# Kernel tuning notes

Measured on AMD Instinct MI355X. Metric: run time of the kernel, lower is better.

The kernel has to match this reference:

```python
import jax, jax.numpy as jnp
import numpy as np

N_NODES = 100000
N_EDGES = 1250000
D_FEAT = 64


def setup_inputs() -> dict:
    key = jax.random.key(0)
    kx, ke = jax.random.split(key)
    x = jax.random.normal(kx, (N_NODES, D_FEAT), dtype=jnp.float32)
    edge_index = jax.random.randint(ke, (2, N_EDGES), 0, N_NODES, dtype=jnp.int64)
    return {"x": x, "edge_index": edge_index}


def _aggregate(x, src, dst, num_nodes):
    # out[i] = sum_{e: dst[e]==i} x[src[e]]  (identity message, 'add' aggr)
    return jax.ops.segment_sum(x[src], dst, num_segments=num_nodes)


def reference(x, edge_index):
    num_nodes = x.shape[0]
    src, dst = edge_index[0], edge_index[1]  # PyG source_to_target flow
    h = _aggregate(x, src, dst, num_nodes)   # conv1
    h = jax.nn.relu(h)
    h = _aggregate(h, src, dst, num_nodes)   # conv2
    return h
```

## Files before the change

### kernel.cpp

```cpp
#include <hip/hip_runtime.h>
#include <hip/hip_bf16.h>


#define N_FEAT   64
#define B_SHIFT  6
#define NPB      64
#define CAPB     1024
#define HALF_CAP 512
#define NLOC     32
#define NB_H     1568
#define GSTRIDE  16
#define TILE     4096

typedef unsigned int u32;
typedef unsigned short u16;
typedef __attribute__((ext_vector_type(8))) unsigned short u16x8;
typedef __attribute__((ext_vector_type(4))) unsigned int u32x4;
typedef __attribute__((ext_vector_type(2))) float f32x2;

__device__ inline u16 f2bf(float f) {
    u32 u = __builtin_bit_cast(u32, f);
    return (u16)((u + 0x7FFFu + ((u >> 16) & 1u)) >> 16);
}

__global__ __launch_bounds__(256) void partition_convert_kernel(
    const float* __restrict__ xf, u16* __restrict__ xb, int n_elems,
    const int* __restrict__ src, const int* __restrict__ dst,
    u32* __restrict__ gcur,
    u32* __restrict__ bdata,
    int n_edges, int n_buckets, int part_blocks)
{
    __shared__ u32 hist[NB_H];
    __shared__ u32 wcur[NB_H];

    const int tid = threadIdx.x;

    if ((int)blockIdx.x >= part_blocks) {
        int i = (((int)blockIdx.x - part_blocks) * 256 + tid) * 8;
        if (i < n_elems) {
            float4 a = *(const float4*)(xf + i);
            float4 b = *(const float4*)(xf + i + 4);
            u16x8 r;
            r[0]=f2bf(a.x); r[1]=f2bf(a.y); r[2]=f2bf(a.z); r[3]=f2bf(a.w);
            r[4]=f2bf(b.x); r[5]=f2bf(b.y); r[6]=f2bf(b.z); r[7]=f2bf(b.w);
            *(u16x8*)(xb + i) = r;
        }
        return;
    }

    const int tbase = (int)blockIdx.x * TILE;
    const int tend  = min(tbase + TILE, n_edges);

    for (int i = tid; i < NB_H; i += 256) hist[i] = 0;
    __syncthreads();

    for (int e = tbase + tid; e < tend; e += 256)
        atomicAdd(&hist[(u32)dst[e] >> B_SHIFT], 1u);
    __syncthreads();

    for (int b = tid; b < n_buckets; b += 256) {
        u32 h = hist[b];
        if (h) wcur[b] = atomicAdd(&gcur[b * GSTRIDE], h);
    }
    __syncthreads();

    for (int e = tbase + tid; e < tend; e += 256) {
        int d = dst[e];
        int s = src[e];
        u32 b   = (u32)d >> B_SHIFT;
        u32 pos = atomicAdd(&wcur[b], 1u);
        if (pos < CAPB)
            bdata[(size_t)b * CAPB + pos] = ((u32)(d & (NPB - 1)) << 17) | (u32)s;
    }
}

__global__ __launch_bounds__(256) void aggregate_kernel(
    const u16* __restrict__ xin,
    const u32* __restrict__ gcur,
    const u32* __restrict__ bdata,
    u16* __restrict__ out_bf,
    float* __restrict__ out_f,
    int n_nodes, int pass)
{
    __shared__ u32 ebuf[HALF_CAP];
    __shared__ u32 sorted[HALF_CAP];
    __shared__ u32 lcnt[NLOC];
    __shared__ u32 lpos[NLOC];
    __shared__ int ptr[NLOC + 1];
    __shared__ u32 ecnt;

    const int tid  = threadIdx.x;
    const int B    = blockIdx.x >> 1;
    const int half = blockIdx.x & 1;

    if (tid < NLOC) { lcnt[tid] = 0; lpos[tid] = 0; }
    if (tid == 0) ecnt = 0;
    __syncthreads();

    int cnt = (int)gcur[B * GSTRIDE];
    if (cnt > CAPB) cnt = CAPB;

    const u32* bd = bdata + (size_t)B * CAPB;
    for (int j = tid; j < cnt; j += 256) {
        u32 p  = bd[j];
        int dl = (int)(p >> 17);
        if ((dl >> 5) == half) {
            u32 pos = atomicAdd(&ecnt, 1u);
            if (pos < HALF_CAP) {
                ebuf[pos] = p;
                atomicAdd(&lcnt[dl & (NLOC - 1)], 1u);
            }
        }
    }
    __syncthreads();

    if (tid < NLOC) {
        int sc = (int)lcnt[tid];
        #pragma unroll
        for (int d = 1; d < NLOC; d <<= 1) {
            int o = __shfl_up(sc, d);
            if (tid >= d) sc += o;
        }
        ptr[tid + 1] = sc;
        if (tid == 0) ptr[0] = 0;
    }
    __syncthreads();

    int en = (int)ecnt; if (en > HALF_CAP) en = HALF_CAP;
    for (int j = tid; j < en; j += 256) {
        u32 p  = ebuf[j];
        int dl = (int)(p >> 17) & (NLOC - 1);
        u32 pos = atomicAdd(&lpos[dl], 1u);
        sorted[ptr[dl] + pos] = p & 0x1FFFFu;
    }
    __syncthreads();

    const int w    = tid >> 6;
    const int lane = tid & 63;
    const int grp  = lane >> 3;
    const int sub  = lane & 7;
    const char* xc = (const char*)xin;

    const int nl   = w * 8 + grp;
    const int node = B * NPB + half * NLOC + nl;
    const int s0 = ptr[nl], s1 = ptr[nl + 1];

    f32x2 a0={0.f,0.f}, a1={0.f,0.f}, a2={0.f,0.f}, a3={0.f,0.f};
    for (int j = s0; j < s1; ++j) {
        u32 s = sorted[j];
        u32x4 v = *(const u32x4*)(xc + ((size_t)s << 7) + (sub << 4));
        a0 += (f32x2){ __builtin_bit_cast(float, v[0] << 16),
                       __builtin_bit_cast(float, v[0] & 0xFFFF0000u) };
        a1 += (f32x2){ __builtin_bit_cast(float, v[1] << 16),
                       __builtin_bit_cast(float, v[1] & 0xFFFF0000u) };
        a2 += (f32x2){ __builtin_bit_cast(float, v[2] << 16),
                       __builtin_bit_cast(float, v[2] & 0xFFFF0000u) };
        a3 += (f32x2){ __builtin_bit_cast(float, v[3] << 16),
                       __builtin_bit_cast(float, v[3] & 0xFFFF0000u) };
    }

    if (node < n_nodes) {
        if (pass == 0) {
            u16x8 o;
            o[0]=f2bf(fmaxf(a0.x,0.f)); o[1]=f2bf(fmaxf(a0.y,0.f));
            o[2]=f2bf(fmaxf(a1.x,0.f)); o[3]=f2bf(fmaxf(a1.y,0.f));
            o[4]=f2bf(fmaxf(a2.x,0.f)); o[5]=f2bf(fmaxf(a2.y,0.f));
            o[6]=f2bf(fmaxf(a3.x,0.f)); o[7]=f2bf(fmaxf(a3.y,0.f));
            *(u16x8*)(out_bf + (size_t)node * N_FEAT + sub * 8) = o;
        } else {
            float* dp = out_f + (size_t)node * N_FEAT + sub * 8;
            *(float4*)dp       = (float4){a0.x, a0.y, a1.x, a1.y};
            *(float4*)(dp + 4) = (float4){a2.x, a2.y, a3.x, a3.y};
        }
    }
}

extern "C" void kernel_launch(void* const* d_in, const int* in_sizes, int n_in,
                              void* d_out, int out_size, void* d_ws, size_t ws_size,
                              hipStream_t stream) {
    const float* x          = (const float*)d_in[0];
    const int*   edge_index = (const int*)d_in[1];

    const int n_edges = in_sizes[1] / 2;
    const int* src = edge_index;
    const int* dst = edge_index + n_edges;

    const int n_nodes   = out_size / N_FEAT;
    const int n_buckets = (n_nodes + NPB - 1) >> B_SHIFT;
    float* out = (float*)d_out;

    const size_t xb_bytes    = (size_t)out_size * sizeof(u16);
    const size_t hb_bytes    = (size_t)out_size * sizeof(u16);
    const size_t bdata_bytes = (size_t)n_buckets * CAPB * sizeof(u32);
    const size_t gcur_bytes  = (size_t)NB_H * GSTRIDE * sizeof(u32);

    char* w = (char*)d_ws;
    u16* xb    = (u16*)w;                w += xb_bytes;
    u16* hb    = (u16*)w;                w += hb_bytes;
    u32* bdata = (u32*)w;                w += bdata_bytes;
    u32* gcur  = (u32*)w;

    hipMemsetAsync(gcur, 0, gcur_bytes, stream);

    const int part_blocks = (n_edges + TILE - 1) / TILE;
    const int conv_blocks = (out_size / 8 + 255) / 256;
    partition_convert_kernel<<<part_blocks + conv_blocks, 256, 0, stream>>>(
        x, xb, out_size, src, dst, gcur, bdata, n_edges, n_buckets, part_blocks);

    const int agg_blocks = 2 * n_buckets;
    aggregate_kernel<<<agg_blocks, 256, 0, stream>>>(xb, gcur, bdata, hb, nullptr, n_nodes, 0);
    aggregate_kernel<<<agg_blocks, 256, 0, stream>>>(hb, gcur, bdata, nullptr, out, n_nodes, 1);
}
```

Before: 178.3 us.

## Sort edge bins once into CSR and reuse in both aggregation passes

Adds a bin_sort_kernel that sorts each 128-node bin's edges by destination once and writes per-node pointers, so both aggregation passes read a ready CSR instead of re-partitioning and sorting in shared memory each time. Bins grow to 128 nodes with larger tiles, and the global-cursor atomics are issued in a rotated order per block to spread contention. The aggregate loop loads eight source ids cooperatively and broadcasts them with shuffles. This costs an extra kernel launch and an extra pass over the edge data, and relies on the larger bin capacity of 2048 not overflowing.

```diff
diff --git a/kernel.cpp b/kernel.cpp
--- a/kernel.cpp
+++ b/kernel.cpp
@@ -2,15 +2,14 @@
 #include <hip/hip_bf16.h>
 
 
-#define N_FEAT   64
-#define B_SHIFT  6
-#define NPB      64
-#define CAPB     1024
-#define HALF_CAP 512
-#define NLOC     32
-#define NB_H     1568
-#define GSTRIDE  16
-#define TILE     4096
+#define N_FEAT    64
+#define BIN_SHIFT 7
+#define BIN_NODES 128
+#define CAPBIN    2048
+#define NB_H      784
+#define GSTRIDE   16
+#define TILE      8192
+#define NPTR      (BIN_NODES + 1)
 
 typedef unsigned int u32;
 typedef unsigned short u16;
@@ -27,8 +26,8 @@
     const float* __restrict__ xf, u16* __restrict__ xb, int n_elems,
     const int* __restrict__ src, const int* __restrict__ dst,
     u32* __restrict__ gcur,
-    u32* __restrict__ bdata,
-    int n_edges, int n_buckets, int part_blocks)
+    u32* __restrict__ cbdata,
+    int n_edges, int n_bins, int part_blocks)
 {
     __shared__ u32 hist[NB_H];
     __shared__ u32 wcur[NB_H];
@@ -55,10 +54,12 @@
     __syncthreads();
 
     for (int e = tbase + tid; e < tend; e += 256)
-        atomicAdd(&hist[(u32)dst[e] >> B_SHIFT], 1u);
-    __syncthreads();
-
-    for (int b = tid; b < n_buckets; b += 256) {
+        atomicAdd(&hist[(u32)dst[e] >> BIN_SHIFT], 1u);
+    __syncthreads();
+
+    const int rot = (int)(((u32)blockIdx.x * 193u) % (u32)n_bins);
+    for (int i = tid; i < n_bins; i += 256) {
+        int b = i + rot; if (b >= n_bins) b -= n_bins;
         u32 h = hist[b];
         if (h) wcur[b] = atomicAdd(&gcur[b * GSTRIDE], h);
     }
@@ -67,73 +68,80 @@
     for (int e = tbase + tid; e < tend; e += 256) {
         int d = dst[e];
         int s = src[e];
-        u32 b   = (u32)d >> B_SHIFT;
+        u32 b   = (u32)d >> BIN_SHIFT;
         u32 pos = atomicAdd(&wcur[b], 1u);
-        if (pos < CAPB)
-            bdata[(size_t)b * CAPB + pos] = ((u32)(d & (NPB - 1)) << 17) | (u32)s;
-    }
+        if (pos < CAPBIN)
+            cbdata[(size_t)b * CAPBIN + pos] =
+                ((u32)(d & (BIN_NODES - 1)) << 17) | (u32)s;
+    }
+}
+
+__global__ __launch_bounds__(256) void bin_sort_kernel(
+    u32* __restrict__ cbdata,
+    const u32* __restrict__ gcur,
+    u32* __restrict__ nodeptr,
+    int n_bins)
+{
+    __shared__ u32 hist[BIN_NODES];
+    __shared__ u32 ptrs[NPTR];
+    __shared__ u32 lpos[BIN_NODES];
+    __shared__ u32 sl[CAPBIN];
+
+    const int tid = threadIdx.x;
+    const int bin = blockIdx.x;
+    if (bin >= n_bins) return;
+
+    if (tid < BIN_NODES) { hist[tid] = 0; lpos[tid] = 0; }
+    __syncthreads();
+
+    int cnt = (int)gcur[bin * GSTRIDE];
+    if (cnt > CAPBIN) cnt = CAPBIN;
+    u32* bd = cbdata + (size_t)bin * CAPBIN;
+
+    for (int j = tid; j < cnt; j += 256)
+        atomicAdd(&hist[bd[j] >> 17], 1u);
+    __syncthreads();
+
+    if (tid < 64) {
+        u32 a = hist[2 * tid], b = hist[2 * tid + 1];
+        u32 s = a + b;
+        #pragma unroll
+        for (int d = 1; d < 64; d <<= 1) {
+            u32 o = __shfl_up(s, d);
+            if (tid >= d) s += o;
+        }
+        ptrs[2 * tid]     = s - a - b;
+        ptrs[2 * tid + 1] = s - b;
+        if (tid == 63) ptrs[BIN_NODES] = s;
+    }
+    __syncthreads();
+
+    for (int j = tid; j < cnt; j += 256) {
+        u32 p   = bd[j];
+        u32 nid = p >> 17;
+        u32 pos = ptrs[nid] + atomicAdd(&lpos[nid], 1u);
+        sl[pos] = p & 0x1FFFFu;
+    }
+    __syncthreads();
+
+    const u32 base = (u32)bin * CAPBIN;
+    for (int j = tid; j < cnt; j += 256)
+        bd[j] = sl[j];
+    if (tid < NPTR)
+        nodeptr[(size_t)bin * NPTR + tid] = base + ptrs[tid];
 }
 
 __global__ __launch_bounds__(256) void aggregate_kernel(
     const u16* __restrict__ xin,
-    const u32* __restrict__ gcur,
-    const u32* __restrict__ bdata,
+    const u32* __restrict__ csorted,
+    const u32* __restrict__ nodeptr,
     u16* __restrict__ out_bf,
     float* __restrict__ out_f,
     int n_nodes, int pass)
 {
-    __shared__ u32 ebuf[HALF_CAP];
-    __shared__ u32 sorted[HALF_CAP];
-    __shared__ u32 lcnt[NLOC];
-    __shared__ u32 lpos[NLOC];
-    __shared__ int ptr[NLOC + 1];
-    __shared__ u32 ecnt;
-
     const int tid  = threadIdx.x;
     const int B    = blockIdx.x >> 1;
     const int half = blockIdx.x & 1;
-
-    if (tid < NLOC) { lcnt[tid] = 0; lpos[tid] = 0; }
-    if (tid == 0) ecnt = 0;
-    __syncthreads();
-
-    int cnt = (int)gcur[B * GSTRIDE];
-    if (cnt > CAPB) cnt = CAPB;
-
-    const u32* bd = bdata + (size_t)B * CAPB;
-    for (int j = tid; j < cnt; j += 256) {
-        u32 p  = bd[j];
-        int dl = (int)(p >> 17);
-        if ((dl >> 5) == half) {
-            u32 pos = atomicAdd(&ecnt, 1u);
-            if (pos < HALF_CAP) {
-                ebuf[pos] = p;
-                atomicAdd(&lcnt[dl & (NLOC - 1)], 1u);
-            }
-        }
-    }
-    __syncthreads();
-
-    if (tid < NLOC) {
-        int sc = (int)lcnt[tid];
-        #pragma unroll
-        for (int d = 1; d < NLOC; d <<= 1) {
-            int o = __shfl_up(sc, d);
-            if (tid >= d) sc += o;
-        }
-        ptr[tid + 1] = sc;
-        if (tid == 0) ptr[0] = 0;
-    }
-    __syncthreads();
-
-    int en = (int)ecnt; if (en > HALF_CAP) en = HALF_CAP;
-    for (int j = tid; j < en; j += 256) {
-        u32 p  = ebuf[j];
-        int dl = (int)(p >> 17) & (NLOC - 1);
-        u32 pos = atomicAdd(&lpos[dl], 1u);
-        sorted[ptr[dl] + pos] = p & 0x1FFFFu;
-    }
-    __syncthreads();
 
     const int w    = tid >> 6;
     const int lane = tid & 63;
@@ -142,21 +150,32 @@
     const char* xc = (const char*)xin;
 
     const int nl   = w * 8 + grp;
-    const int node = B * NPB + half * NLOC + nl;
-    const int s0 = ptr[nl], s1 = ptr[nl + 1];
+    const int node = B * 64 + half * 32 + nl;
+
+    const int bin = node >> BIN_SHIFT;
+    const int nid = node & (BIN_NODES - 1);
+    const int s0  = (int)nodeptr[(size_t)bin * NPTR + nid];
+    const int s1  = (int)nodeptr[(size_t)bin * NPTR + nid + 1];
 
     f32x2 a0={0.f,0.f}, a1={0.f,0.f}, a2={0.f,0.f}, a3={0.f,0.f};
-    for (int j = s0; j < s1; ++j) {
-        u32 s = sorted[j];
-        u32x4 v = *(const u32x4*)(xc + ((size_t)s << 7) + (sub << 4));
-        a0 += (f32x2){ __builtin_bit_cast(float, v[0] << 16),
-                       __builtin_bit_cast(float, v[0] & 0xFFFF0000u) };
-        a1 += (f32x2){ __builtin_bit_cast(float, v[1] << 16),
-                       __builtin_bit_cast(float, v[1] & 0xFFFF0000u) };
-        a2 += (f32x2){ __builtin_bit_cast(float, v[2] << 16),
-                       __builtin_bit_cast(float, v[2] & 0xFFFF0000u) };
-        a3 += (f32x2){ __builtin_bit_cast(float, v[3] << 16),
-                       __builtin_bit_cast(float, v[3] & 0xFFFF0000u) };
+
+    for (int jb = s0; jb < s1; jb += 8) {
+        u32 myid = 0;
+        if (jb + sub < s1) myid = csorted[jb + sub];
+        const int m = min(8, s1 - jb);
+        #pragma unroll 1
+        for (int k = 0; k < m; ++k) {
+            u32 s = (u32)__shfl((int)myid, (lane & 56) + k, 64);
+            u32x4 v = *(const u32x4*)(xc + ((size_t)s << 7) + (sub << 4));
+            a0 += (f32x2){ __builtin_bit_cast(float, v[0] << 16),
+                           __builtin_bit_cast(float, v[0] & 0xFFFF0000u) };
+            a1 += (f32x2){ __builtin_bit_cast(float, v[1] << 16),
+                           __builtin_bit_cast(float, v[1] & 0xFFFF0000u) };
+            a2 += (f32x2){ __builtin_bit_cast(float, v[2] << 16),
+                           __builtin_bit_cast(float, v[2] & 0xFFFF0000u) };
+            a3 += (f32x2){ __builtin_bit_cast(float, v[3] << 16),
+                           __builtin_bit_cast(float, v[3] & 0xFFFF0000u) };
+        }
     }
 
     if (node < n_nodes) {
@@ -185,29 +204,33 @@
     const int* src = edge_index;
     const int* dst = edge_index + n_edges;
 
-    const int n_nodes   = out_size / N_FEAT;
-    const int n_buckets = (n_nodes + NPB - 1) >> B_SHIFT;
+    const int n_nodes = out_size / N_FEAT;
+    const int n_bins  = (n_nodes + BIN_NODES - 1) >> BIN_SHIFT;
     float* out = (float*)d_out;
 
     const size_t xb_bytes    = (size_t)out_size * sizeof(u16);
     const size_t hb_bytes    = (size_t)out_size * sizeof(u16);
-    const size_t bdata_bytes = (size_t)n_buckets * CAPB * sizeof(u32);
+    const size_t cb_bytes    = (size_t)n_bins * CAPBIN * sizeof(u32);
+    const size_t np_bytes    = (size_t)n_bins * NPTR * sizeof(u32);
     const size_t gcur_bytes  = (size_t)NB_H * GSTRIDE * sizeof(u32);
 
     char* w = (char*)d_ws;
-    u16* xb    = (u16*)w;                w += xb_bytes;
-    u16* hb    = (u16*)w;                w += hb_bytes;
-    u32* bdata = (u32*)w;                w += bdata_bytes;
-    u32* gcur  = (u32*)w;
+    u16* xb      = (u16*)w;              w += xb_bytes;
+    u16* hb      = (u16*)w;              w += hb_bytes;
+    u32* cbdata  = (u32*)w;              w += cb_bytes;
+    u32* nodeptr = (u32*)w;              w += np_bytes;
+    u32* gcur    = (u32*)w;
 
     hipMemsetAsync(gcur, 0, gcur_bytes, stream);
 
     const int part_blocks = (n_edges + TILE - 1) / TILE;
     const int conv_blocks = (out_size / 8 + 255) / 256;
     partition_convert_kernel<<<part_blocks + conv_blocks, 256, 0, stream>>>(
-        x, xb, out_size, src, dst, gcur, bdata, n_edges, n_buckets, part_blocks);
-
-    const int agg_blocks = 2 * n_buckets;
-    aggregate_kernel<<<agg_blocks, 256, 0, stream>>>(xb, gcur, bdata, hb, nullptr, n_nodes, 0);
-    aggregate_kernel<<<agg_blocks, 256, 0, stream>>>(hb, gcur, bdata, nullptr, out, n_nodes, 1);
-}
+        x, xb, out_size, src, dst, gcur, cbdata, n_edges, n_bins, part_blocks);
+
+    bin_sort_kernel<<<n_bins, 256, 0, stream>>>(cbdata, gcur, nodeptr, n_bins);
+
+    const int agg_blocks = 2 * ((n_nodes + 63) / 64);
+    aggregate_kernel<<<agg_blocks, 256, 0, stream>>>(xb, cbdata, nodeptr, hb, nullptr, n_nodes, 0);
+    aggregate_kernel<<<agg_blocks, 256, 0, stream>>>(hb, cbdata, nodeptr, nullptr, out, n_nodes, 1);
+}
```

Result: slower. 186.1 us (+4.4%).
